# Kernel optimization log

Measured on AMD Instinct MI355X. Metric: run time of the kernel, lower is better.

Reference implementation:

```python
import jax, jax.numpy as jnp
import numpy as np

N_NODES = 50000
N_EDGES = 1600000
D_FEAT = 32


def setup_inputs() -> dict:
    key = jax.random.key(0)
    k1, k2, k3, k4 = jax.random.split(key, 4)
    node_feat = jax.random.normal(k1, (N_NODES, D_FEAT), dtype=jnp.float32)
    edge_feat = jax.random.normal(k2, (N_EDGES, D_FEAT), dtype=jnp.float32)
    eps = jnp.zeros((1,), dtype=jnp.float32)  # learnable eps, init 0
    src = jax.random.randint(k3, (N_EDGES,), 0, N_NODES, dtype=jnp.int64)
    dst = jax.random.randint(k4, (N_EDGES,), 0, N_NODES, dtype=jnp.int64)
    return {"node_feat": node_feat, "edge_feat": edge_feat, "eps": eps,
            "src": src, "dst": dst}


def reference(node_feat, edge_feat, eps, src, dst):
    # message: relu(h_src + h_edge) per edge  [E, D]
    m = jax.nn.relu(node_feat[src] + edge_feat)
    # sum-aggregate messages into destination nodes  [N, D]
    neigh = jax.ops.segment_sum(m, dst, num_segments=node_feat.shape[0])
    # eps-scaled residual
    return (1.0 + eps[0]) * node_feat + neigh
```

## Files before the change

### kernel.cpp

```cpp
#include <hip/hip_runtime.h>

#define N_NODES 50000
#define N_EDGES 1600000
#define D_FEAT 32
#define SCAN_BLOCK 1024
#define N_SCAN_BLOCKS ((N_NODES + SCAN_BLOCK - 1) / SCAN_BLOCK)
#define NPART 8
#define PART_SIZE ((N_NODES + NPART - 1) / NPART)
#define SCATTER_BLOCKS 2048

#define WS_CNT   0
#define WS_EXCL  (N_NODES)
#define WS_OM    (2 * N_NODES)
#define WS_BSUM  (3 * N_NODES)
#define WS_BSUMX (3 * N_NODES + 64)
#define WS_PAIR  (3 * N_NODES + 128)

typedef float f4 __attribute__((ext_vector_type(4)));


__global__ void hist(const int* __restrict__ dst, int* __restrict__ cnt) {
    int q = blockIdx.x * blockDim.x + threadIdx.x;
    const int NQ = N_EDGES / 4;
    if (q >= NQ) return;
    int4 d4 = ((const int4*)dst)[q];
    atomicAdd(&cnt[d4.x], 1);
    atomicAdd(&cnt[d4.y], 1);
    atomicAdd(&cnt[d4.z], 1);
    atomicAdd(&cnt[d4.w], 1);
}

__global__ void scan_blocks(const int* __restrict__ cnt,
                            int* __restrict__ excl,
                            int* __restrict__ bsum) {
    __shared__ int lds[SCAN_BLOCK];
    int tid = threadIdx.x;
    int i = blockIdx.x * SCAN_BLOCK + tid;
    int v = (i < N_NODES) ? cnt[i] : 0;
    int sum = v;
    lds[tid] = v;
    __syncthreads();
    for (int ofs = 1; ofs < SCAN_BLOCK; ofs <<= 1) {
        int t = (tid >= ofs) ? lds[tid - ofs] : 0;
        __syncthreads();
        sum += t;
        lds[tid] = sum;
        __syncthreads();
    }
    if (i < N_NODES) excl[i] = sum - v;
    if (tid == SCAN_BLOCK - 1) bsum[blockIdx.x] = lds[SCAN_BLOCK - 1];
}

__global__ void scan_bsums(const int* __restrict__ bsum, int* __restrict__ bsumx) {
    int lane = threadIdx.x;
    int orig = (lane < N_SCAN_BLOCKS) ? bsum[lane] : 0;
    int v = orig;
    for (int o = 1; o < 64; o <<= 1) {
        int t = __shfl_up(v, o);
        if (lane >= o) v += t;
    }
    if (lane < N_SCAN_BLOCKS) bsumx[lane] = v - orig;
}

__global__ void finalize_off(const int* __restrict__ excl,
                             const int* __restrict__ bsumx,
                             int* __restrict__ om) {
    int i = blockIdx.x * SCAN_BLOCK + threadIdx.x;
    if (i < N_NODES) om[i] = excl[i] + bsumx[blockIdx.x];
}

__global__ void scatter_pairs(const int* __restrict__ src,
                              const int* __restrict__ dst,
                              int* __restrict__ om,
                              int2* __restrict__ pair) {
    int part = blockIdx.x & (NPART - 1);
    int lo = part * PART_SIZE;
    int hi = lo + PART_SIZE;
    int bi = blockIdx.x >> 3;
    const int nb = SCATTER_BLOCKS / NPART;
    const int NQ = N_EDGES / 4;
    for (int q = bi * blockDim.x + threadIdx.x; q < NQ; q += nb * blockDim.x) {
        int4 d4 = ((const int4*)dst)[q];
        int4 s4 = ((const int4*)src)[q];
        int e0 = q * 4;
        if (d4.x >= lo && d4.x < hi) pair[atomicAdd(&om[d4.x], 1)] = make_int2(e0,     s4.x);
        if (d4.y >= lo && d4.y < hi) pair[atomicAdd(&om[d4.y], 1)] = make_int2(e0 + 1, s4.y);
        if (d4.z >= lo && d4.z < hi) pair[atomicAdd(&om[d4.z], 1)] = make_int2(e0 + 2, s4.z);
        if (d4.w >= lo && d4.w < hi) pair[atomicAdd(&om[d4.w], 1)] = make_int2(e0 + 3, s4.w);
    }
}

__global__ void reduce_gather(const float* __restrict__ node_feat,
                              const float* __restrict__ edge_feat,
                              const float* __restrict__ eps,
                              const int* __restrict__ excl,
                              const int* __restrict__ bsumx,
                              const int* __restrict__ cnt,
                              const int2* __restrict__ pair,
                              float* __restrict__ out) {
    int t = blockIdx.x * blockDim.x + threadIdx.x;
    int n = t >> 3;
    int g = t & 7;
    if (n >= N_NODES) return;

    int start = excl[n] + bsumx[n >> 10];
    int c = cnt[n];
    int gbase = (threadIdx.x & 63) & ~7;

    const f4* efp = (const f4*)edge_feat;
    const f4* nfp = (const f4*)node_feat;

    f4 acc = (f4)(0.f);

    int idx0 = start + g;
    if (idx0 > N_EDGES - 1) idx0 = N_EDGES - 1;
    int2 p = pair[idx0];

    for (int i0 = 0; i0 < c; i0 += 8) {
        int idxn = start + i0 + 8 + g;
        if (idxn > N_EDGES - 1) idxn = N_EDGES - 1;
        int2 pn = pair[idxn];

        int lim = c - i0;
        if (lim > 8) lim = 8;
#pragma unroll
        for (int j = 0; j < 8; ++j) {
            if (j < lim) {
                int e = __shfl(p.x, gbase + j);
                int s = __shfl(p.y, gbase + j);
                f4 ef = __builtin_nontemporal_load(&efp[(size_t)e * 8 + g]);
                f4 nf = nfp[(size_t)s * 8 + g];
                acc.x += fmaxf(nf.x + ef.x, 0.f);
                acc.y += fmaxf(nf.y + ef.y, 0.f);
                acc.z += fmaxf(nf.z + ef.z, 0.f);
                acc.w += fmaxf(nf.w + ef.w, 0.f);
            }
        }
        p = pn;
    }

    float scale = 1.0f + eps[0];
    f4 h = nfp[(size_t)n * 8 + g];
    f4 o;
    o.x = scale * h.x + acc.x;
    o.y = scale * h.y + acc.y;
    o.z = scale * h.z + acc.z;
    o.w = scale * h.w + acc.w;
    ((f4*)out)[(size_t)n * 8 + g] = o;
}


__global__ void fb_init_out(const float* __restrict__ node_feat,
                            const float* __restrict__ eps,
                            float* __restrict__ out) {
    int i = blockIdx.x * blockDim.x + threadIdx.x;
    const int n4 = N_NODES * D_FEAT / 4;
    float scale = 1.0f + eps[0];
    if (i < n4) {
        float4 v = ((const float4*)node_feat)[i];
        v.x *= scale; v.y *= scale; v.z *= scale; v.w *= scale;
        ((float4*)out)[i] = v;
    }
}

__global__ void fb_scatter(const float* __restrict__ node_feat,
                           const float* __restrict__ edge_feat,
                           const int* __restrict__ src,
                           const int* __restrict__ dst,
                           float* __restrict__ out) {
    int t = blockIdx.x * blockDim.x + threadIdx.x;
    int e = t >> 3;
    int g = t & 7;
    if (e >= N_EDGES) return;
    int s = src[e];
    int d = dst[e];
    float4 nf = ((const float4*)node_feat)[s * 8 + g];
    float4 ef = ((const float4*)edge_feat)[(size_t)e * 8 + g];
    float* op = out + (size_t)d * D_FEAT + g * 4;
    unsafeAtomicAdd(op + 0, fmaxf(nf.x + ef.x, 0.f));
    unsafeAtomicAdd(op + 1, fmaxf(nf.y + ef.y, 0.f));
    unsafeAtomicAdd(op + 2, fmaxf(nf.z + ef.z, 0.f));
    unsafeAtomicAdd(op + 3, fmaxf(nf.w + ef.w, 0.f));
}

extern "C" void kernel_launch(void* const* d_in, const int* in_sizes, int n_in,
                              void* d_out, int out_size, void* d_ws, size_t ws_size,
                              hipStream_t stream) {
    const float* node_feat = (const float*)d_in[0];
    const float* edge_feat = (const float*)d_in[1];
    const float* eps       = (const float*)d_in[2];
    const int*   src       = (const int*)d_in[3];
    const int*   dst       = (const int*)d_in[4];
    float* out = (float*)d_out;

    const int B = 256;
    const size_t need = ((size_t)WS_PAIR + 2ull * N_EDGES) * sizeof(int);

    if (ws_size < need) {
        int n4 = N_NODES * D_FEAT / 4;
        fb_init_out<<<(n4 + B - 1) / B, B, 0, stream>>>(node_feat, eps, out);
        long long total = (long long)N_EDGES * 8;
        fb_scatter<<<(int)((total + B - 1) / B), B, 0, stream>>>(
            node_feat, edge_feat, src, dst, out);
        return;
    }

    int* ws = (int*)d_ws;
    int*  cnt   = ws + WS_CNT;
    int*  excl  = ws + WS_EXCL;
    int*  om    = ws + WS_OM;
    int*  bsum  = ws + WS_BSUM;
    int*  bsumx = ws + WS_BSUMX;
    int2* pair  = (int2*)(ws + WS_PAIR);

    hipMemsetAsync(cnt, 0, N_NODES * sizeof(int), stream);

    int nq = N_EDGES / 4;
    hist<<<(nq + B - 1) / B, B, 0, stream>>>(dst, cnt);
    scan_blocks<<<N_SCAN_BLOCKS, SCAN_BLOCK, 0, stream>>>(cnt, excl, bsum);
    scan_bsums<<<1, 64, 0, stream>>>(bsum, bsumx);
    finalize_off<<<N_SCAN_BLOCKS, SCAN_BLOCK, 0, stream>>>(excl, bsumx, om);

    scatter_pairs<<<SCATTER_BLOCKS, B, 0, stream>>>(src, dst, om, pair);

    long long ntotal = (long long)N_NODES * 8;
    reduce_gather<<<(int)((ntotal + B - 1) / B), B, 0, stream>>>(
        node_feat, edge_feat, eps, excl, bsumx, cnt, pair, out);
}
```

Measured before the change: 465.7 us.

## Scatter only edge ids and gather src in reduce, drop partitioned scatter

The CSR build now writes only the edge id per sorted slot instead of an (edge, src) pair, and the scatter runs as one single pass over all edges rather than eight destination-range passes. The reduce kernel looks up src through the edge id, which adds a dependent random load per edge. The loop is split into full 8-edge chunks plus a remainder, dropping the per-iteration bound checks and the prefetch of the next chunk. This halves the scatter's write traffic and avoids rereading dst eight times, at the cost of less locality in the scatter atomics and an extra indirection in the gather.

Measured after the change: 532.8 us. +14.4%, slower.

```diff
diff --git a/kernel.cpp b/kernel.cpp
--- a/kernel.cpp
+++ b/kernel.cpp
@@ -5,16 +5,13 @@
 #define D_FEAT 32
 #define SCAN_BLOCK 1024
 #define N_SCAN_BLOCKS ((N_NODES + SCAN_BLOCK - 1) / SCAN_BLOCK)
-#define NPART 8
-#define PART_SIZE ((N_NODES + NPART - 1) / NPART)
-#define SCATTER_BLOCKS 2048
 
 #define WS_CNT   0
 #define WS_EXCL  (N_NODES)
 #define WS_OM    (2 * N_NODES)
 #define WS_BSUM  (3 * N_NODES)
 #define WS_BSUMX (3 * N_NODES + 64)
-#define WS_PAIR  (3 * N_NODES + 128)
+#define WS_EID   (3 * N_NODES + 128)
 
 typedef float f4 __attribute__((ext_vector_type(4)));
 
@@ -69,34 +66,28 @@
     if (i < N_NODES) om[i] = excl[i] + bsumx[blockIdx.x];
 }
 
-__global__ void scatter_pairs(const int* __restrict__ src,
-                              const int* __restrict__ dst,
-                              int* __restrict__ om,
-                              int2* __restrict__ pair) {
-    int part = blockIdx.x & (NPART - 1);
-    int lo = part * PART_SIZE;
-    int hi = lo + PART_SIZE;
-    int bi = blockIdx.x >> 3;
-    const int nb = SCATTER_BLOCKS / NPART;
+__global__ void scatter_eid(const int* __restrict__ dst,
+                            int* __restrict__ om,
+                            int* __restrict__ eid) {
+    int q = blockIdx.x * blockDim.x + threadIdx.x;
     const int NQ = N_EDGES / 4;
-    for (int q = bi * blockDim.x + threadIdx.x; q < NQ; q += nb * blockDim.x) {
-        int4 d4 = ((const int4*)dst)[q];
-        int4 s4 = ((const int4*)src)[q];
-        int e0 = q * 4;
-        if (d4.x >= lo && d4.x < hi) pair[atomicAdd(&om[d4.x], 1)] = make_int2(e0,     s4.x);
-        if (d4.y >= lo && d4.y < hi) pair[atomicAdd(&om[d4.y], 1)] = make_int2(e0 + 1, s4.y);
-        if (d4.z >= lo && d4.z < hi) pair[atomicAdd(&om[d4.z], 1)] = make_int2(e0 + 2, s4.z);
-        if (d4.w >= lo && d4.w < hi) pair[atomicAdd(&om[d4.w], 1)] = make_int2(e0 + 3, s4.w);
-    }
+    if (q >= NQ) return;
+    int4 d4 = ((const int4*)dst)[q];
+    int e0 = q * 4;
+    eid[atomicAdd(&om[d4.x], 1)] = e0;
+    eid[atomicAdd(&om[d4.y], 1)] = e0 + 1;
+    eid[atomicAdd(&om[d4.z], 1)] = e0 + 2;
+    eid[atomicAdd(&om[d4.w], 1)] = e0 + 3;
 }
 
 __global__ void reduce_gather(const float* __restrict__ node_feat,
                               const float* __restrict__ edge_feat,
                               const float* __restrict__ eps,
+                              const int* __restrict__ src,
                               const int* __restrict__ excl,
                               const int* __restrict__ bsumx,
                               const int* __restrict__ cnt,
-                              const int2* __restrict__ pair,
+                              const int* __restrict__ eid,
                               float* __restrict__ out) {
     int t = blockIdx.x * blockDim.x + threadIdx.x;
     int n = t >> 3;
@@ -111,32 +102,36 @@
     const f4* nfp = (const f4*)node_feat;
 
     f4 acc = (f4)(0.f);
-
-    int idx0 = start + g;
-    if (idx0 > N_EDGES - 1) idx0 = N_EDGES - 1;
-    int2 p = pair[idx0];
-
-    for (int i0 = 0; i0 < c; i0 += 8) {
-        int idxn = start + i0 + 8 + g;
-        if (idxn > N_EDGES - 1) idxn = N_EDGES - 1;
-        int2 pn = pair[idxn];
-
-        int lim = c - i0;
-        if (lim > 8) lim = 8;
+    int i0 = 0;
+    for (; i0 + 8 <= c; i0 += 8) {
+        int p  = eid[start + i0 + g];
+        int sv = src[p];
 #pragma unroll
         for (int j = 0; j < 8; ++j) {
-            if (j < lim) {
-                int e = __shfl(p.x, gbase + j);
-                int s = __shfl(p.y, gbase + j);
-                f4 ef = __builtin_nontemporal_load(&efp[(size_t)e * 8 + g]);
-                f4 nf = nfp[(size_t)s * 8 + g];
-                acc.x += fmaxf(nf.x + ef.x, 0.f);
-                acc.y += fmaxf(nf.y + ef.y, 0.f);
-                acc.z += fmaxf(nf.z + ef.z, 0.f);
-                acc.w += fmaxf(nf.w + ef.w, 0.f);
-            }
+            int e = __shfl(p,  gbase + j);
+            int s = __shfl(sv, gbase + j);
+            f4 ef = __builtin_nontemporal_load(&efp[(size_t)e * 8 + g]);
+            f4 nf = nfp[(size_t)s * 8 + g];
+            acc.x += fmaxf(nf.x + ef.x, 0.f);
+            acc.y += fmaxf(nf.y + ef.y, 0.f);
+            acc.z += fmaxf(nf.z + ef.z, 0.f);
+            acc.w += fmaxf(nf.w + ef.w, 0.f);
         }
-        p = pn;
+    }
+    int rem = c - i0;
+    if (rem > 0) {
+        int p  = (g < rem) ? eid[start + i0 + g] : 0;
+        int sv = src[p];
+        for (int j = 0; j < rem; ++j) {
+            int e = __shfl(p,  gbase + j);
+            int s = __shfl(sv, gbase + j);
+            f4 ef = __builtin_nontemporal_load(&efp[(size_t)e * 8 + g]);
+            f4 nf = nfp[(size_t)s * 8 + g];
+            acc.x += fmaxf(nf.x + ef.x, 0.f);
+            acc.y += fmaxf(nf.y + ef.y, 0.f);
+            acc.z += fmaxf(nf.z + ef.z, 0.f);
+            acc.w += fmaxf(nf.w + ef.w, 0.f);
+        }
     }
 
     float scale = 1.0f + eps[0];
@@ -194,7 +189,7 @@
     float* out = (float*)d_out;
 
     const int B = 256;
-    const size_t need = ((size_t)WS_PAIR + 2ull * N_EDGES) * sizeof(int);
+    const size_t need = ((size_t)WS_EID + (size_t)N_EDGES) * sizeof(int);
 
     if (ws_size < need) {
         int n4 = N_NODES * D_FEAT / 4;
@@ -211,7 +206,7 @@
     int*  om    = ws + WS_OM;
     int*  bsum  = ws + WS_BSUM;
     int*  bsumx = ws + WS_BSUMX;
-    int2* pair  = (int2*)(ws + WS_PAIR);
+    int*  eid   = ws + WS_EID;
 
     hipMemsetAsync(cnt, 0, N_NODES * sizeof(int), stream);
 
@@ -221,9 +216,9 @@
     scan_bsums<<<1, 64, 0, stream>>>(bsum, bsumx);
     finalize_off<<<N_SCAN_BLOCKS, SCAN_BLOCK, 0, stream>>>(excl, bsumx, om);
 
-    scatter_pairs<<<SCATTER_BLOCKS, B, 0, stream>>>(src, dst, om, pair);
+    scatter_eid<<<(nq + B - 1) / B, B, 0, stream>>>(dst, om, eid);
 
     long long ntotal = (long long)N_NODES * 8;
     reduce_gather<<<(int)((ntotal + B - 1) / B), B, 0, stream>>>(
-        node_feat, edge_feat, eps, excl, bsumx, cnt, pair, out);
-}
+        node_feat, edge_feat, eps, src, excl, bsumx, cnt, eid, out);
+}
```
